# Performance work log

Measured on AMD Instinct MI355X. Metric: run time of the kernel, lower is better.

## Reference

```python
import jax, jax.numpy as jnp
import numpy as np

DIM = 1024
HEADS = 16
HEAD_DIM = DIM // HEADS
EPS = 1e-5
THETA = 10000.0


def _rope(t):
    # t: (b, s, d). lucidrains rotary: interleaved pairs, full-dim rotation, theta=10000.
    b, s, d = t.shape
    inv_freq = 1.0 / (THETA ** (jnp.arange(0, d, 2, dtype=jnp.float32) / d))  # (d/2,)
    ang = jnp.arange(s, dtype=jnp.float32)[:, None] * inv_freq[None, :]        # (s, d/2)
    cos, sin = jnp.cos(ang), jnp.sin(ang)
    tp = t.reshape(b, s, d // 2, 2)
    x1, x2 = tp[..., 0], tp[..., 1]
    o1 = x1 * cos - x2 * sin
    o2 = x2 * cos + x1 * sin
    return jnp.stack([o1, o2], axis=-1).reshape(b, s, d)


def setup_inputs() -> dict:
    key = jax.random.key(0)
    ks = jax.random.split(key, 10)
    b, s, d = 2, 2048, DIM
    scale = 1.0 / np.sqrt(d)
    return {
        "x": jax.random.normal(ks[0], (b, s, d), dtype=jnp.float32),
        "mask": jax.random.normal(ks[1], (b, s, s), dtype=jnp.float32),
        "ln_g": jnp.ones((d,), dtype=jnp.float32),
        "ln_b": jnp.zeros((d,), dtype=jnp.float32),
        "w_qkv": jax.random.normal(ks[2], (3 * d, d), dtype=jnp.float32) * scale,
        "b_qkv": jnp.zeros((3 * d,), dtype=jnp.float32),
        "in_w": jax.random.normal(ks[3], (3 * d, d), dtype=jnp.float32) * scale,
        "in_b": jnp.zeros((3 * d,), dtype=jnp.float32),
        "out_w": jax.random.normal(ks[4], (d, d), dtype=jnp.float32) * scale,
        "out_b": jnp.zeros((d,), dtype=jnp.float32),
    }


def reference(x, mask, ln_g, ln_b, w_qkv, b_qkv, in_w, in_b, out_w, out_b):
    b, s, d = x.shape
    # LayerNorm
    mu = jnp.mean(x, axis=-1, keepdims=True)
    var = jnp.mean((x - mu) ** 2, axis=-1, keepdims=True)
    xn = (x - mu) * jax.lax.rsqrt(var + EPS) * ln_g + ln_b
    # fused qkv projection, then chunk
    qkv = xn @ w_qkv.T + b_qkv
    q, k, v = jnp.split(qkv, 3, axis=-1)
    # RoPE on q, k (full dim, interleaved pairs)
    q = _rope(q)
    k = _rope(k)
    # nn.MultiheadAttention re-applies its own in-projection
    wq, wk, wv = jnp.split(in_w, 3, axis=0)
    bq, bk, bv = jnp.split(in_b, 3, axis=0)
    def to_heads(t, w, bias):
        t = t @ w.T + bias
        return t.reshape(b, s, HEADS, HEAD_DIM).transpose(0, 2, 1, 3)  # (b,h,s,hd)
    qh = to_heads(q, wq, bq)
    kh = to_heads(k, wk, bk)
    vh = to_heads(v, wv, bv)
    scores = jnp.einsum('bhid,bhjd->bhij', qh, kh) / np.sqrt(HEAD_DIM)
    scores = scores + mask[:, None, :, :]  # mask repeated over heads
    attn = jax.nn.softmax(scores, axis=-1)
    out = jnp.einsum('bhij,bhjd->bhid', attn, vh)
    out = out.transpose(0, 2, 1, 3).reshape(b, s, d)
    return out @ out_w.T + out_b
```

## Files before the change

### kernel.cpp

```cpp
#include <hip/hip_runtime.h>

using u16 = unsigned short;
using u32 = unsigned int;
typedef __attribute__((ext_vector_type(8))) short short8;
typedef __attribute__((ext_vector_type(4))) float f32x4;

#define LOG2E 1.4426950408889634f
#define SCALE2 0.18033688011112042f

__device__ __forceinline__ u16 f2b(float f) {
  union { float f; unsigned u; } v; v.f = f;
  unsigned r = v.u + 0x7fffu + ((v.u >> 16) & 1u);
  return (u16)(r >> 16);
}

__device__ __forceinline__ void wg_barrier() {
  asm volatile("s_waitcnt lgkmcnt(0)\n\ts_barrier" ::: "memory");
}

__global__ __launch_bounds__(256) void prep(const float* __restrict__ w_qkv, u16* __restrict__ wqkv_b,
                                            const float* __restrict__ in_w, u16* __restrict__ inw_b,
                                            const float* __restrict__ out_w, u16* __restrict__ outw_b,
                                            float2* __restrict__ rtab,
                                            const float* __restrict__ mask, u16* __restrict__ maskp,
                                            const float* __restrict__ x,
                                            const float* __restrict__ ln_g,
                                            const float* __restrict__ ln_b,
                                            u16* __restrict__ xn) {
  __shared__ u16 T[128 * 68];
  __shared__ float sbuf[4], ssbuf[4];
  int blk = blockIdx.x, t = threadIdx.x;
  if (blk < 7168) {
    int i = blk * 256 + t;
    const float* s; u16* d; int off;
    if (i < 786432)       { s = w_qkv; d = wqkv_b; off = i; }
    else if (i < 1572864) { s = in_w;  d = inw_b;  off = i - 786432; }
    else                  { s = out_w; d = outw_b; off = i - 1572864; }
    float4 v = ((const float4*)s)[off];
    uint2 o;
    o.x = (unsigned)f2b(v.x) | ((unsigned)f2b(v.y) << 16);
    o.y = (unsigned)f2b(v.z) | ((unsigned)f2b(v.w) << 16);
    ((uint2*)d)[off] = o;
  } else if (blk < 11264) {
    int idx = (blk - 7168) * 256 + t;
    int pos = idx >> 9, i = idx & 511;
    float ifreq = exp2f(-(float)(2 * i) * (13.287712379549449f / 1024.0f));
    float ang = (float)pos * ifreq;
    rtab[idx] = make_float2(__cosf(ang), __sinf(ang));
  } else if (blk < 12288) {
    int mb = blk - 11264;
    int kt = mb & 31, qt = (mb >> 5) & 15, bb = mb >> 9;
    const float* src = mask + ((size_t)bb * 2048 + qt * 128) * 2048 + kt * 64;
    #pragma unroll
    for (int it = 0; it < 8; it++) {
      int id = it * 256 + t;
      int r = id >> 4, c4 = (id & 15) * 4;
      float4 v = *(const float4*)(src + (size_t)r * 2048 + c4);
      T[r * 68 + c4 + 0] = f2b(v.x * LOG2E);
      T[r * 68 + c4 + 1] = f2b(v.y * LOG2E);
      T[r * 68 + c4 + 2] = f2b(v.z * LOG2E);
      T[r * 68 + c4 + 3] = f2b(v.w * LOG2E);
    }
    __syncthreads();
    size_t obase = (size_t)(((bb * 16 + qt) * 32) + kt) * 8192;
    #pragma unroll
    for (int it = 0; it < 2; it++) {
      int pos = it * 256 + t;
      int l15 = pos & 15, g = pos >> 4;
      int w = g >> 3, p = (g >> 2) & 1, qd = g & 3;
      int qlocal = w * 32 + p * 16 + l15;
      u16 vals[16];
      #pragma unroll
      for (int mt = 0; mt < 4; mt++)
        #pragma unroll
        for (int reg = 0; reg < 4; reg++)
          vals[mt * 4 + reg] = T[qlocal * 68 + mt * 16 + qd * 4 + reg];
      uint4* dst = (uint4*)(maskp + obase + (size_t)pos * 16);
      dst[0] = *(uint4*)&vals[0];
      dst[1] = *(uint4*)&vals[8];
    }
  } else {
    int row = blk - 12288;
    const float* xr = x + (size_t)row * 1024;
    float4 v = *(const float4*)(xr + t * 4);
    float s = v.x + v.y + v.z + v.w;
    float ss = v.x * v.x + v.y * v.y + v.z * v.z + v.w * v.w;
    #pragma unroll
    for (int m = 1; m < 64; m <<= 1) {
      s  += __shfl_xor(s, m);
      ss += __shfl_xor(ss, m);
    }
    int wave = t >> 6, lane = t & 63;
    if (lane == 0) { sbuf[wave] = s; ssbuf[wave] = ss; }
    __syncthreads();
    s  = sbuf[0] + sbuf[1] + sbuf[2] + sbuf[3];
    ss = ssbuf[0] + ssbuf[1] + ssbuf[2] + ssbuf[3];
    float mean = s * (1.0f / 1024.0f);
    float var  = ss * (1.0f / 1024.0f) - mean * mean;
    float rstd = 1.0f / sqrtf(var + 1e-5f);
    float4 gv = *(const float4*)(ln_g + t * 4);
    float4 bv = *(const float4*)(ln_b + t * 4);
    uint2 o;
    o.x = (unsigned)f2b((v.x - mean) * rstd * gv.x + bv.x) |
          ((unsigned)f2b((v.y - mean) * rstd * gv.y + bv.y) << 16);
    o.y = (unsigned)f2b((v.z - mean) * rstd * gv.z + bv.z) |
          ((unsigned)f2b((v.w - mean) * rstd * gv.w + bv.w) << 16);
    *(uint2*)(xn + (size_t)row * 1024 + t * 4) = o;
  }
}

template<bool SLAB, bool OUT_BF16, bool ROPE>
__global__ __launch_bounds__(256, 3) void gemm_pipe(const u16* __restrict__ A, int lda,
                                                    const u16* __restrict__ W,
                                                    const float* __restrict__ bias,
                                                    const float2* __restrict__ rtab,
                                                    float* __restrict__ Cf,
                                                    u16* __restrict__ Cb,
                                                    int ldc, int K) {
  __shared__ u16 As[2][128 * 36];
  __shared__ u16 Bs[2][128 * 36];
  int n0 = blockIdx.x * 128, m0 = blockIdx.y * 128;
  int aoff = SLAB ? ((n0 >> 10) << 10) : 0;
  int tid = threadIdx.x;
  int lane = tid & 63, l15 = lane & 15, quad = lane >> 4;
  int w = tid >> 6, mw = w & 1, nw = w >> 1;
  const u16* Abase = A + (size_t)m0 * lda + aoff;
  const u16* Wbase = W + (size_t)n0 * K;
  int r0 = tid >> 2;
  int c4 = (tid & 3) * 8;
  f32x4 acc[4][4];
  #pragma unroll
  for (int i = 0; i < 4; i++)
    #pragma unroll
    for (int j = 0; j < 4; j++) acc[i][j] = (f32x4){0.f, 0.f, 0.f, 0.f};

  uint4 a0, a1, w0, w1;
  #define GLOADS(k0)                                                          \
    a0 = *(const uint4*)(Abase + (size_t)(r0)      * lda + (k0) + c4);        \
    a1 = *(const uint4*)(Abase + (size_t)(r0 + 64) * lda + (k0) + c4);        \
    w0 = *(const uint4*)(Wbase + (size_t)(r0)      * K   + (k0) + c4);        \
    w1 = *(const uint4*)(Wbase + (size_t)(r0 + 64) * K   + (k0) + c4);
  #define LSTORES(b)                                                          \
    *(uint4*)&As[b][(r0)      * 36 + c4] = a0;                                \
    *(uint4*)&As[b][(r0 + 64) * 36 + c4] = a1;                                \
    *(uint4*)&Bs[b][(r0)      * 36 + c4] = w0;                                \
    *(uint4*)&Bs[b][(r0 + 64) * 36 + c4] = w1;

  GLOADS(0);
  LSTORES(0);
  if (K > 32) { GLOADS(32); }
  wg_barrier();
  for (int k0 = 0; k0 < K; k0 += 32) {
    int b = (k0 >> 5) & 1;
    if (k0 + 32 < K) { LSTORES(b ^ 1); }
    if (k0 + 64 < K) { GLOADS(k0 + 64); }
    short8 af[4], bfr[4];
    #pragma unroll
    for (int mt = 0; mt < 4; mt++)
      af[mt] = *(const short8*)&As[b][(mw * 64 + mt * 16 + l15) * 36 + quad * 8];
    #pragma unroll
    for (int nt = 0; nt < 4; nt++)
      bfr[nt] = *(const short8*)&Bs[b][(nw * 64 + nt * 16 + l15) * 36 + quad * 8];
    #pragma unroll
    for (int mt = 0; mt < 4; mt++)
      #pragma unroll
      for (int nt = 0; nt < 4; nt++)
        acc[mt][nt] = __builtin_amdgcn_mfma_f32_16x16x32_bf16(
            af[mt], bfr[nt], acc[mt][nt], 0, 0, 0);
    wg_barrier();
  }
  #undef GLOADS
  #undef LSTORES
  int mb = m0 + mw * 64, nb = n0 + nw * 64;
  float bv[4];
  #pragma unroll
  for (int nt = 0; nt < 4; nt++) bv[nt] = bias[nb + nt * 16 + l15];
  #pragma unroll
  for (int mt = 0; mt < 4; mt++)
    #pragma unroll
    for (int nt = 0; nt < 4; nt++) {
      int col = nb + nt * 16 + l15;
      #pragma unroll
      for (int reg = 0; reg < 4; reg++) {
        int row = mb + mt * 16 + quad * 4 + reg;
        float val = acc[mt][nt][reg] + bv[nt];
        if (ROPE && col < 2048) {
          float pr = __shfl_xor(val, 1);
          float2 cs = rtab[(size_t)(row & 2047) * 512 + ((col & 1023) >> 1)];
          val = (col & 1) ? fmaf(val, cs.x, pr * cs.y)
                          : fmaf(val, cs.x, -pr * cs.y);
        }
        if (OUT_BF16) Cb[(size_t)row * ldc + col] = f2b(val);
        else          Cf[(size_t)row * ldc + col] = val;
      }
    }
}

__global__ __launch_bounds__(256) void transpose_v(const u16* __restrict__ qkv2,
                                                   u16* __restrict__ vT) {
  __shared__ u16 T[64 * 72];
  int st = blockIdx.x, h = blockIdx.y, bb = blockIdx.z;
  int t = threadIdx.x;
  int r = t >> 2, c0 = (t & 3) * 16;
  const u16* src = qkv2 + (size_t)(bb * 2048 + st * 64 + r) * 3072 + 2048 + h * 64 + c0;
  *(uint4*)&T[r * 72 + c0]     = *(const uint4*)src;
  *(uint4*)&T[r * 72 + c0 + 8] = *(const uint4*)(src + 8);
  __syncthreads();
  int d = t >> 2, s0 = (t & 3) * 16;
  u16 tmp[16];
  #pragma unroll
  for (int j = 0; j < 16; j++) tmp[j] = T[(s0 + j) * 72 + d];
  u16* dst = vT + ((size_t)((bb * 16 + h) * 64 + d)) * 2048 + st * 64 + s0;
  *(uint4*)dst       = *(uint4*)&tmp[0];
  *(uint4*)(dst + 8) = *(uint4*)&tmp[8];
}

__global__ __launch_bounds__(256) void attn_mfma(const u16* __restrict__ qkv2,
                                                 const u16* __restrict__ vT,
                                                 const u16* __restrict__ maskp,
                                                 u16* __restrict__ attn_out) {
  __shared__ u16 Kb[2][64 * 72];
  __shared__ u16 Vb[2][64 * 72];
  __shared__ u16 Ps[128 * 72];
  int h = blockIdx.x, qt = blockIdx.y, bb = blockIdx.z;
  int tid = threadIdx.x;
  int lane = tid & 63, l15 = lane & 15, quad = lane >> 4;
  int w = tid >> 6;
  int sr = tid >> 2, sc = (tid & 3) * 16;
  const u16* kslab = qkv2 + ((size_t)bb * 2048) * 3072 + 1024 + h * 64;
  const u16* vslab = vT + ((size_t)((bb * 16 + h) * 64)) * 2048;

  {
    int r = w * 32 + (lane >> 1), c0 = (lane & 1) * 32;
    const u16* src = qkv2 + (size_t)(bb * 2048 + qt * 128 + r) * 3072 + h * 64 + c0;
    #pragma unroll
    for (int u = 0; u < 4; u++)
      *(uint4*)&Ps[r * 72 + c0 + u * 8] = *(const uint4*)(src + u * 8);
  }
  {
    const u16* ks = kslab + (size_t)sr * 3072 + sc;
    const u16* vs = vslab + (size_t)sr * 2048 + sc;
    *(uint4*)&Kb[0][sr * 72 + sc]     = *(const uint4*)ks;
    *(uint4*)&Kb[0][sr * 72 + sc + 8] = *(const uint4*)(ks + 8);
    *(uint4*)&Vb[0][sr * 72 + sc]     = *(const uint4*)vs;
    *(uint4*)&Vb[0][sr * 72 + sc + 8] = *(const uint4*)(vs + 8);
  }
  short8 bq[2][2];
  #pragma unroll
  for (int p = 0; p < 2; p++)
    #pragma unroll
    for (int hk = 0; hk < 2; hk++)
      bq[p][hk] = *(const short8*)&Ps[(w * 32 + p * 16 + l15) * 72 + hk * 32 + quad * 8];
  float lsum[2] = {0.f, 0.f};
  f32x4 acc[2][4];
  #pragma unroll
  for (int p = 0; p < 2; p++)
    #pragma unroll
    for (int dt = 0; dt < 4; dt++) acc[p][dt] = (f32x4){0.f, 0.f, 0.f, 0.f};
  const u16* mtile = maskp + ((size_t)((bb * 16 + qt) * 32)) * 8192
                     + (((w * 2) * 4 + quad) * 16 + l15) * 16;
  wg_barrier();

  for (int kt = 0; kt < 32; kt++) {
    int b = kt & 1;
    uint4 mA[2], mB[2];
    {
      const u16* mt_ = mtile + (size_t)kt * 8192;
      #pragma unroll
      for (int p = 0; p < 2; p++) {
        const uint4* mq = (const uint4*)(mt_ + p * 1024);
        mA[p] = mq[0]; mB[p] = mq[1];
      }
    }
    uint4 kr0, kr1, vr0, vr1;
    if (kt + 1 < 32) {
      const u16* ks = kslab + (size_t)((kt + 1) * 64 + sr) * 3072 + sc;
      const u16* vs = vslab + (size_t)sr * 2048 + (kt + 1) * 64 + sc;
      kr0 = *(const uint4*)ks; kr1 = *(const uint4*)(ks + 8);
      vr0 = *(const uint4*)vs; vr1 = *(const uint4*)(vs + 8);
    }
    short8 ak[4][2];
    #pragma unroll
    for (int mt = 0; mt < 4; mt++)
      #pragma unroll
      for (int hk = 0; hk < 2; hk++)
        ak[mt][hk] = *(const short8*)&Kb[b][(mt * 16 + l15) * 72 + hk * 32 + quad * 8];
    #pragma unroll
    for (int p = 0; p < 2; p++) {
      f32x4 st[4];
      #pragma unroll
      for (int mt = 0; mt < 4; mt++) {
        f32x4 z = (f32x4){0.f, 0.f, 0.f, 0.f};
        z = __builtin_amdgcn_mfma_f32_16x16x32_bf16(ak[mt][0], bq[p][0], z, 0, 0, 0);
        st[mt] = __builtin_amdgcn_mfma_f32_16x16x32_bf16(ak[mt][1], bq[p][1], z, 0, 0, 0);
      }
      u32 wds[8] = {mA[p].x, mA[p].y, mA[p].z, mA[p].w, mB[p].x, mB[p].y, mB[p].z, mB[p].w};
      float mv[16];
      #pragma unroll
      for (int j = 0; j < 8; j++) {
        mv[2 * j]     = __uint_as_float(wds[j] << 16);
        mv[2 * j + 1] = __uint_as_float(wds[j] & 0xffff0000u);
      }
      int prow = (w * 32 + p * 16 + l15) * 72 + quad * 4;
      #pragma unroll
      for (int mt = 0; mt < 4; mt++) {
        u32 pk0, pk1;
        float sv0 = fmaf(st[mt][0], SCALE2, mv[mt * 4 + 0]);
        float sv1 = fmaf(st[mt][1], SCALE2, mv[mt * 4 + 1]);
        float sv2 = fmaf(st[mt][2], SCALE2, mv[mt * 4 + 2]);
        float sv3 = fmaf(st[mt][3], SCALE2, mv[mt * 4 + 3]);
        float p0 = __builtin_amdgcn_exp2f(sv0), p1 = __builtin_amdgcn_exp2f(sv1);
        float p2 = __builtin_amdgcn_exp2f(sv2), p3 = __builtin_amdgcn_exp2f(sv3);
        lsum[p] += (p0 + p1) + (p2 + p3);
        pk0 = ((__float_as_uint(p0) + 0x8000u) >> 16) |
              ((__float_as_uint(p1) + 0x8000u) & 0xffff0000u);
        pk1 = ((__float_as_uint(p2) + 0x8000u) >> 16) |
              ((__float_as_uint(p3) + 0x8000u) & 0xffff0000u);
        *(uint2*)&Ps[prow + mt * 16] = make_uint2(pk0, pk1);
      }
    }
    short8 ap[2][2];
    #pragma unroll
    for (int p = 0; p < 2; p++)
      #pragma unroll
      for (int hk = 0; hk < 2; hk++)
        ap[p][hk] = *(const short8*)&Ps[(w * 32 + p * 16 + l15) * 72 + hk * 32 + quad * 8];
    #pragma unroll
    for (int dt = 0; dt < 4; dt++) {
      short8 bv0 = *(const short8*)&Vb[b][(dt * 16 + l15) * 72 + quad * 8];
      short8 bv1 = *(const short8*)&Vb[b][(dt * 16 + l15) * 72 + 32 + quad * 8];
      #pragma unroll
      for (int p = 0; p < 2; p++) {
        acc[p][dt] = __builtin_amdgcn_mfma_f32_16x16x32_bf16(ap[p][0], bv0, acc[p][dt], 0, 0, 0);
        acc[p][dt] = __builtin_amdgcn_mfma_f32_16x16x32_bf16(ap[p][1], bv1, acc[p][dt], 0, 0, 0);
      }
    }
    if (kt + 1 < 32) {
      int nb = b ^ 1;
      *(uint4*)&Kb[nb][sr * 72 + sc]     = kr0;
      *(uint4*)&Kb[nb][sr * 72 + sc + 8] = kr1;
      *(uint4*)&Vb[nb][sr * 72 + sc]     = vr0;
      *(uint4*)&Vb[nb][sr * 72 + sc + 8] = vr1;
    }
    wg_barrier();
  }
  #pragma unroll
  for (int p = 0; p < 2; p++) {
    float l = lsum[p];
    l += __shfl_xor(l, 16);
    l += __shfl_xor(l, 32);
    #pragma unroll
    for (int reg = 0; reg < 4; reg++) {
      float lq = __shfl(l, quad * 4 + reg);
      float inv = 1.0f / lq;
      int grow = bb * 2048 + qt * 128 + w * 32 + p * 16 + quad * 4 + reg;
      #pragma unroll
      for (int dt = 0; dt < 4; dt++)
        attn_out[(size_t)grow * 1024 + h * 64 + dt * 16 + l15] = f2b(acc[p][dt][reg] * inv);
    }
  }
}

extern "C" void kernel_launch(void* const* d_in, const int* in_sizes, int n_in,
                              void* d_out, int out_size, void* d_ws, size_t ws_size,
                              hipStream_t stream) {
  const float* x     = (const float*)d_in[0];
  const float* mask  = (const float*)d_in[1];
  const float* ln_g  = (const float*)d_in[2];
  const float* ln_b  = (const float*)d_in[3];
  const float* w_qkv = (const float*)d_in[4];
  const float* b_qkv = (const float*)d_in[5];
  const float* in_w  = (const float*)d_in[6];
  const float* in_b  = (const float*)d_in[7];
  const float* out_w = (const float*)d_in[8];
  const float* out_b = (const float*)d_in[9];
  float* out = (float*)d_out;
  char* ws = (char*)d_ws;

  u16* wqkv_b = (u16*)(ws);
  u16* inw_b  = (u16*)(ws + 6291456ull);
  u16* outw_b = (u16*)(ws + 12582912ull);
  u16* xn_b   = (u16*)(ws + 14680064ull);
  u16* attn_b = xn_b;
  u16* qkv_b  = (u16*)(ws + 23068672ull);
  u16* qkv2_b = (u16*)(ws + 48234496ull);
  float2* rtab = (float2*)qkv2_b;
  u16* vT     = (u16*)(ws + 73400320ull);
  u16* maskp  = (u16*)(ws + 81788928ull);

  prep<<<16384, 256, 0, stream>>>(w_qkv, wqkv_b, in_w, inw_b, out_w, outw_b,
                                  rtab, mask, maskp, x, ln_g, ln_b, xn_b);
  gemm_pipe<false, true, true><<<dim3(24, 32), 256, 0, stream>>>(
      xn_b, 1024, wqkv_b, b_qkv, rtab, nullptr, qkv_b, 3072, 1024);
  gemm_pipe<true, true, false><<<dim3(24, 32), 256, 0, stream>>>(
      qkv_b, 3072, inw_b, in_b, nullptr, nullptr, qkv2_b, 3072, 1024);
  transpose_v<<<dim3(32, 16, 2), 256, 0, stream>>>(qkv2_b, vT);
  attn_mfma<<<dim3(16, 16, 2), 256, 0, stream>>>(qkv2_b, vT, maskp, attn_b);
  gemm_pipe<false, false, false><<<dim3(8, 32), 256, 0, stream>>>(
      attn_b, 1024, outw_b, out_b, nullptr, out, nullptr, 1024, 1024);
}
```

Baseline: 310.6 us.

## Fuse V transpose into in-projection GEMM epilogue and deepen load prefetch

Measured after the change: 302.4 us. 2.6% less time.

```diff
diff --git a/kernel.cpp b/kernel.cpp
--- a/kernel.cpp
+++ b/kernel.cpp
@@ -109,13 +109,14 @@
   }
 }
 
-template<bool SLAB, bool OUT_BF16, bool ROPE>
+template<bool SLAB, bool OUT_BF16, bool ROPE, bool WVT>
 __global__ __launch_bounds__(256, 3) void gemm_pipe(const u16* __restrict__ A, int lda,
                                                     const u16* __restrict__ W,
                                                     const float* __restrict__ bias,
                                                     const float2* __restrict__ rtab,
                                                     float* __restrict__ Cf,
                                                     u16* __restrict__ Cb,
+                                                    u16* __restrict__ vT,
                                                     int ldc, int K) {
   __shared__ u16 As[2][128 * 36];
   __shared__ u16 Bs[2][128 * 36];
@@ -135,42 +136,64 @@
     for (int j = 0; j < 4; j++) acc[i][j] = (f32x4){0.f, 0.f, 0.f, 0.f};
 
   uint4 a0, a1, w0, w1;
-  #define GLOADS(k0)                                                          \
+  uint4 b0, b1, x0, x1;
+  #define GLOADS_A(k0)                                                        \
     a0 = *(const uint4*)(Abase + (size_t)(r0)      * lda + (k0) + c4);        \
     a1 = *(const uint4*)(Abase + (size_t)(r0 + 64) * lda + (k0) + c4);        \
     w0 = *(const uint4*)(Wbase + (size_t)(r0)      * K   + (k0) + c4);        \
     w1 = *(const uint4*)(Wbase + (size_t)(r0 + 64) * K   + (k0) + c4);
-  #define LSTORES(b)                                                          \
-    *(uint4*)&As[b][(r0)      * 36 + c4] = a0;                                \
-    *(uint4*)&As[b][(r0 + 64) * 36 + c4] = a1;                                \
-    *(uint4*)&Bs[b][(r0)      * 36 + c4] = w0;                                \
-    *(uint4*)&Bs[b][(r0 + 64) * 36 + c4] = w1;
-
-  GLOADS(0);
-  LSTORES(0);
-  if (K > 32) { GLOADS(32); }
+  #define GLOADS_B(k0)                                                        \
+    b0 = *(const uint4*)(Abase + (size_t)(r0)      * lda + (k0) + c4);        \
+    b1 = *(const uint4*)(Abase + (size_t)(r0 + 64) * lda + (k0) + c4);        \
+    x0 = *(const uint4*)(Wbase + (size_t)(r0)      * K   + (k0) + c4);        \
+    x1 = *(const uint4*)(Wbase + (size_t)(r0 + 64) * K   + (k0) + c4);
+  #define LSTORES_A(bf)                                                       \
+    *(uint4*)&As[bf][(r0)      * 36 + c4] = a0;                               \
+    *(uint4*)&As[bf][(r0 + 64) * 36 + c4] = a1;                               \
+    *(uint4*)&Bs[bf][(r0)      * 36 + c4] = w0;                               \
+    *(uint4*)&Bs[bf][(r0 + 64) * 36 + c4] = w1;
+  #define LSTORES_B(bf)                                                       \
+    *(uint4*)&As[bf][(r0)      * 36 + c4] = b0;                               \
+    *(uint4*)&As[bf][(r0 + 64) * 36 + c4] = b1;                               \
+    *(uint4*)&Bs[bf][(r0)      * 36 + c4] = x0;                               \
+    *(uint4*)&Bs[bf][(r0 + 64) * 36 + c4] = x1;
+  #define COMPUTE(bf)                                                         \
+    {                                                                         \
+      short8 af[4], bfr[4];                                                   \
+      _Pragma("unroll")                                                       \
+      for (int mt = 0; mt < 4; mt++)                                          \
+        af[mt] = *(const short8*)&As[bf][(mw * 64 + mt * 16 + l15) * 36 + quad * 8]; \
+      _Pragma("unroll")                                                       \
+      for (int nt = 0; nt < 4; nt++)                                          \
+        bfr[nt] = *(const short8*)&Bs[bf][(nw * 64 + nt * 16 + l15) * 36 + quad * 8]; \
+      _Pragma("unroll")                                                       \
+      for (int mt = 0; mt < 4; mt++)                                          \
+        _Pragma("unroll")                                                     \
+        for (int nt = 0; nt < 4; nt++)                                        \
+          acc[mt][nt] = __builtin_amdgcn_mfma_f32_16x16x32_bf16(              \
+              af[mt], bfr[nt], acc[mt][nt], 0, 0, 0);                         \
+    }
+
+  GLOADS_A(0);
+  LSTORES_A(0);
+  GLOADS_A(32);
+  GLOADS_B(64);
   wg_barrier();
-  for (int k0 = 0; k0 < K; k0 += 32) {
-    int b = (k0 >> 5) & 1;
-    if (k0 + 32 < K) { LSTORES(b ^ 1); }
-    if (k0 + 64 < K) { GLOADS(k0 + 64); }
-    short8 af[4], bfr[4];
-    #pragma unroll
-    for (int mt = 0; mt < 4; mt++)
-      af[mt] = *(const short8*)&As[b][(mw * 64 + mt * 16 + l15) * 36 + quad * 8];
-    #pragma unroll
-    for (int nt = 0; nt < 4; nt++)
-      bfr[nt] = *(const short8*)&Bs[b][(nw * 64 + nt * 16 + l15) * 36 + quad * 8];
-    #pragma unroll
-    for (int mt = 0; mt < 4; mt++)
-      #pragma unroll
-      for (int nt = 0; nt < 4; nt++)
-        acc[mt][nt] = __builtin_amdgcn_mfma_f32_16x16x32_bf16(
-            af[mt], bfr[nt], acc[mt][nt], 0, 0, 0);
+  for (int k0 = 0; k0 < K; k0 += 64) {
+    if (k0 + 32 < K)  { LSTORES_A(1); }
+    if (k0 + 96 < K)  { GLOADS_A(k0 + 96); }
+    COMPUTE(0);
     wg_barrier();
-  }
-  #undef GLOADS
-  #undef LSTORES
+    if (k0 + 64 < K)  { LSTORES_B(0); }
+    if (k0 + 128 < K) { GLOADS_B(k0 + 128); }
+    COMPUTE(1);
+    wg_barrier();
+  }
+  #undef GLOADS_A
+  #undef GLOADS_B
+  #undef LSTORES_A
+  #undef LSTORES_B
+  #undef COMPUTE
   int mb = m0 + mw * 64, nb = n0 + nw * 64;
   float bv[4];
   #pragma unroll
@@ -180,39 +203,30 @@
     #pragma unroll
     for (int nt = 0; nt < 4; nt++) {
       int col = nb + nt * 16 + l15;
-      #pragma unroll
-      for (int reg = 0; reg < 4; reg++) {
-        int row = mb + mt * 16 + quad * 4 + reg;
-        float val = acc[mt][nt][reg] + bv[nt];
-        if (ROPE && col < 2048) {
-          float pr = __shfl_xor(val, 1);
-          float2 cs = rtab[(size_t)(row & 2047) * 512 + ((col & 1023) >> 1)];
-          val = (col & 1) ? fmaf(val, cs.x, pr * cs.y)
-                          : fmaf(val, cs.x, -pr * cs.y);
+      if (WVT && col >= 2048) {
+        int hh = (col - 2048) >> 6, dd = (col - 2048) & 63;
+        int row0 = mb + mt * 16 + quad * 4;
+        int bbi = row0 >> 11, s0 = row0 & 2047;
+        u16 vv[4];
+        #pragma unroll
+        for (int reg = 0; reg < 4; reg++) vv[reg] = f2b(acc[mt][nt][reg] + bv[nt]);
+        *(uint2*)&vT[((size_t)((bbi * 16 + hh) * 64 + dd)) * 2048 + s0] = *(uint2*)vv;
+      } else {
+        #pragma unroll
+        for (int reg = 0; reg < 4; reg++) {
+          int row = mb + mt * 16 + quad * 4 + reg;
+          float val = acc[mt][nt][reg] + bv[nt];
+          if (ROPE && col < 2048) {
+            float pr = __shfl_xor(val, 1);
+            float2 cs = rtab[(size_t)(row & 2047) * 512 + ((col & 1023) >> 1)];
+            val = (col & 1) ? fmaf(val, cs.x, pr * cs.y)
+                            : fmaf(val, cs.x, -pr * cs.y);
+          }
+          if (OUT_BF16) Cb[(size_t)row * ldc + col] = f2b(val);
+          else          Cf[(size_t)row * ldc + col] = val;
         }
-        if (OUT_BF16) Cb[(size_t)row * ldc + col] = f2b(val);
-        else          Cf[(size_t)row * ldc + col] = val;
-      }
-    }
-}
-
-__global__ __launch_bounds__(256) void transpose_v(const u16* __restrict__ qkv2,
-                                                   u16* __restrict__ vT) {
-  __shared__ u16 T[64 * 72];
-  int st = blockIdx.x, h = blockIdx.y, bb = blockIdx.z;
-  int t = threadIdx.x;
-  int r = t >> 2, c0 = (t & 3) * 16;
-  const u16* src = qkv2 + (size_t)(bb * 2048 + st * 64 + r) * 3072 + 2048 + h * 64 + c0;
-  *(uint4*)&T[r * 72 + c0]     = *(const uint4*)src;
-  *(uint4*)&T[r * 72 + c0 + 8] = *(const uint4*)(src + 8);
-  __syncthreads();
-  int d = t >> 2, s0 = (t & 3) * 16;
-  u16 tmp[16];
-  #pragma unroll
-  for (int j = 0; j < 16; j++) tmp[j] = T[(s0 + j) * 72 + d];
-  u16* dst = vT + ((size_t)((bb * 16 + h) * 64 + d)) * 2048 + st * 64 + s0;
-  *(uint4*)dst       = *(uint4*)&tmp[0];
-  *(uint4*)(dst + 8) = *(uint4*)&tmp[8];
+      }
+    }
 }
 
 __global__ __launch_bounds__(256) void attn_mfma(const u16* __restrict__ qkv2,
@@ -390,12 +404,11 @@
 
   prep<<<16384, 256, 0, stream>>>(w_qkv, wqkv_b, in_w, inw_b, out_w, outw_b,
                                   rtab, mask, maskp, x, ln_g, ln_b, xn_b);
-  gemm_pipe<false, true, true><<<dim3(24, 32), 256, 0, stream>>>(
-      xn_b, 1024, wqkv_b, b_qkv, rtab, nullptr, qkv_b, 3072, 1024);
-  gemm_pipe<true, true, false><<<dim3(24, 32), 256, 0, stream>>>(
-      qkv_b, 3072, inw_b, in_b, nullptr, nullptr, qkv2_b, 3072, 1024);
-  transpose_v<<<dim3(32, 16, 2), 256, 0, stream>>>(qkv2_b, vT);
+  gemm_pipe<false, true, true, false><<<dim3(24, 32), 256, 0, stream>>>(
+      xn_b, 1024, wqkv_b, b_qkv, rtab, nullptr, qkv_b, nullptr, 3072, 1024);
+  gemm_pipe<true, true, false, true><<<dim3(24, 32), 256, 0, stream>>>(
+      qkv_b, 3072, inw_b, in_b, nullptr, nullptr, qkv2_b, vT, 3072, 1024);
   attn_mfma<<<dim3(16, 16, 2), 256, 0, stream>>>(qkv2_b, vT, maskp, attn_b);
-  gemm_pipe<false, false, false><<<dim3(8, 32), 256, 0, stream>>>(
-      attn_b, 1024, outw_b, out_b, nullptr, out, nullptr, 1024, 1024);
-}
+  gemm_pipe<false, false, false, false><<<dim3(8, 32), 256, 0, stream>>>(
+      attn_b, 1024, outw_b, out_b, nullptr, out, nullptr, nullptr, 1024, 1024);
+}
```
